# Kernel tuning notes

Measured on AMD Instinct MI355X. Metric: run time of the kernel, lower is better.

## Reference

```python
import jax, jax.numpy as jnp
import numpy as np

B, S, H, NH = 4, 2048, 1024, 16
HD = H // NH  # head_size = 64


def setup_inputs() -> dict:
    key = jax.random.key(0)
    ks = jax.random.split(key, 12)
    s = 1.0 / np.sqrt(H)
    return {
        "query": jax.random.normal(ks[0], (B, S, H), jnp.float32),
        "key": jax.random.normal(ks[1], (B, S, H), jnp.float32),
        "value": jax.random.normal(ks[2], (B, S, H), jnp.float32),
        "attention_mask": jax.random.randint(ks[3], (B, 1, S, S), 0, 2).astype(jnp.float32),
        "Wq": jax.random.normal(ks[4], (H, H), jnp.float32) * s,
        "bq": jnp.zeros((H,), jnp.float32),
        "Wk": jax.random.normal(ks[5], (H, H), jnp.float32) * s,
        "bk": jnp.zeros((H,), jnp.float32),
        "Wv": jax.random.normal(ks[6], (H, H), jnp.float32) * s,
        "bv": jnp.zeros((H,), jnp.float32),
        "Wo": jax.random.normal(ks[7], (H, H), jnp.float32) * s,
        "bo": jnp.zeros((H,), jnp.float32),
    }


def reference(query, key, value, attention_mask, Wq, bq, Wk, bk, Wv, bv, Wo, bo):
    # Linear projections (weights stored [in, out])
    q = query @ Wq + bq   # [B, S, H]
    k = key @ Wk + bk
    v = value @ Wv + bv
    # split heads -> [B, NH, S, HD]
    def heads(x):
        return x.reshape(B, -1, NH, HD).transpose(0, 2, 1, 3)
    q, k, v = heads(q), heads(k), heads(v)
    scale = 1.0 / np.sqrt(HD)
    scores = jnp.einsum("bhqd,bhkd->bhqk", q, k) * scale  # [B, NH, S, S]
    scores = scores + attention_mask * (-1e9)
    attn = jax.nn.softmax(scores, axis=-1)
    # dropout is identity in eval mode (deterministic reference)
    out = jnp.einsum("bhqk,bhkd->bhqd", attn, v)  # [B, NH, S, HD]
    out = out.transpose(0, 2, 1, 3).reshape(B, -1, H)  # [B, S, H]
    return out @ Wo + bo
```

## Files before the change

kernel.cpp:

```cpp
#include <hip/hip_runtime.h>
#include <hip/hip_bf16.h>
#include <stdint.h>

#define B_ 4
#define S_ 2048
#define H_ 1024
#define NH_ 16
#define HD_ 64

typedef __attribute__((ext_vector_type(8))) short short8;
typedef __attribute__((ext_vector_type(4))) float f32x4;
typedef __attribute__((ext_vector_type(4))) unsigned short ushort4v;

__device__ __forceinline__ unsigned short f2bf(float f) {
  union { float f; unsigned u; } x; x.f = f;
  unsigned r = x.u + 0x7fffu + ((x.u >> 16) & 1u);
  return (unsigned short)(r >> 16);
}

#define ALDS16(g, l) \
  __builtin_amdgcn_global_load_lds((const __attribute__((address_space(1))) void*)(g), \
                                   (__attribute__((address_space(3))) void*)(l), 16, 0, 0)

__global__ __launch_bounds__(256) void cvt_in(
    const float* __restrict__ q, const float* __restrict__ k, const float* __restrict__ v,
    unsigned short* __restrict__ oq, unsigned short* __restrict__ ok2, unsigned short* __restrict__ ov) {
  const int z = blockIdx.z;
  const float* src = z == 0 ? q : (z == 1 ? k : v);
  unsigned short* dst = z == 0 ? oq : (z == 1 ? ok2 : ov);
  const size_t i = ((size_t)blockIdx.x * 256 + threadIdx.x) * 8;
  const f32x4 a = *reinterpret_cast<const f32x4*>(src + i);
  const f32x4 c = *reinterpret_cast<const f32x4*>(src + i + 4);
  short8 o;
#pragma unroll
  for (int j = 0; j < 4; ++j) { o[j] = (short)f2bf(a[j]); o[j + 4] = (short)f2bf(c[j]); }
  *reinterpret_cast<short8*>(dst + i) = o;
}

__global__ __launch_bounds__(256) void packmask(
    const float* __restrict__ mask, unsigned long long* __restrict__ mb) {
  const int w = threadIdx.x >> 6, lane = threadIdx.x & 63;
  const int wbase = (blockIdx.x * 4 + w) * 32;
#pragma unroll 8
  for (int i = 0; i < 32; ++i) {
    const float v = mask[(size_t)(wbase + i) * 64 + lane];
    const unsigned long long bits = __ballot(v == 0.0f);
    if (lane == 0) mb[wbase + i] = bits;
  }
}

__global__ __launch_bounds__(256) void cvt_w(
    const float* __restrict__ Wq, const float* __restrict__ Wk,
    const float* __restrict__ Wv, const float* __restrict__ Wo,
    unsigned short* __restrict__ wt) {
  __shared__ float tile[64][65];
  const int z = blockIdx.z;
  const float* W = z == 0 ? Wq : (z == 1 ? Wk : (z == 2 ? Wv : Wo));
  unsigned short* out = wt + (size_t)z * H_ * H_;
  const int t = threadIdx.x;
  const int r0 = blockIdx.y * 64, c0 = blockIdx.x * 64;
  const int tr = t >> 4, tc = (t & 15) * 4;
#pragma unroll
  for (int rr = 0; rr < 4; ++rr) {
    const int row = rr * 16 + tr;
    const f32x4 val = *reinterpret_cast<const f32x4*>(W + (size_t)(r0 + row) * H_ + c0 + tc);
#pragma unroll
    for (int j = 0; j < 4; ++j) tile[row][tc + j] = val[j];
  }
  __syncthreads();
#pragma unroll
  for (int rr = 0; rr < 4; ++rr) {
    const int c = rr * 16 + tr;
    ushort4v o;
#pragma unroll
    for (int j = 0; j < 4; ++j) o[j] = f2bf(tile[tc + j][c]);
    *reinterpret_cast<ushort4v*>(out + (size_t)(c0 + c) * H_ + r0 + tc) = o;
  }
}

template <int OUTMODE>
__device__ __forceinline__ void gemm_body(
    const unsigned short* __restrict__ X, const unsigned short* __restrict__ Wt,
    const float* __restrict__ bias, float oscale, unsigned short* __restrict__ obf,
    float* __restrict__ of32) {
  __shared__ unsigned short As[128 * 64];
  __shared__ unsigned short Bs[128 * 64];
  const int t = threadIdx.x;
  const int w = t >> 6, l = t & 63;
  const int lr = l & 15, lg = l >> 4;
  const int brow = blockIdx.x * 128, bcol = blockIdx.y * 128;
  const int wr = (w >> 1) * 64, wc = (w & 1) * 64;
  f32x4 acc[4][4] = {};
  const unsigned short* xb = X + (size_t)brow * 1024;
  const unsigned short* wb = Wt + (size_t)bcol * 1024;
  int srow[4], skl[4];
#pragma unroll
  for (int j = 0; j < 4; ++j) {
    const int c = t + j * 256;
    srow[j] = c >> 3;
    skl[j] = ((c & 7) ^ ((c >> 3) & 7)) * 8;
  }
  for (int kt = 0; kt < 1024; kt += 64) {
#pragma unroll
    for (int j = 0; j < 4; ++j) {
      ALDS16(xb + (size_t)srow[j] * 1024 + kt + skl[j], As + (t + j * 256) * 8);
      ALDS16(wb + (size_t)srow[j] * 1024 + kt + skl[j], Bs + (t + j * 256) * 8);
    }
    __syncthreads();
#pragma unroll
    for (int kk = 0; kk < 2; ++kk) {
      short8 af[4], bf[4];
#pragma unroll
      for (int m = 0; m < 4; ++m) {
        const int ra = wr + m * 16 + lr;
        af[m] = *reinterpret_cast<const short8*>(As + ra * 64 + ((kk * 4 + lg) ^ (ra & 7)) * 8);
      }
#pragma unroll
      for (int n = 0; n < 4; ++n) {
        const int rb = wc + n * 16 + lr;
        bf[n] = *reinterpret_cast<const short8*>(Bs + rb * 64 + ((kk * 4 + lg) ^ (rb & 7)) * 8);
      }
#pragma unroll
      for (int m = 0; m < 4; ++m)
#pragma unroll
        for (int n = 0; n < 4; ++n)
          acc[m][n] = __builtin_amdgcn_mfma_f32_16x16x32_bf16(af[m], bf[n], acc[m][n], 0, 0, 0);
    }
    __syncthreads();
  }
#pragma unroll
  for (int m = 0; m < 4; ++m) {
#pragma unroll
    for (int n = 0; n < 4; ++n) {
      const int gr0 = brow + wr + m * 16 + lg * 4;
      const int gc = bcol + wc + n * 16 + lr;
      if (OUTMODE == 2) {
        ushort4v o;
#pragma unroll
        for (int r = 0; r < 4; ++r) o[r] = f2bf((acc[m][n][r] + bias[gc]) * oscale);
        const int bb = gr0 >> 11, ss = gr0 & 2047, hh = gc >> 6, dd = gc & 63;
        *reinterpret_cast<ushort4v*>(obf + ((size_t)(bb * NH_ + hh) * HD_ + dd) * S_ + ss) = o;
      } else {
#pragma unroll
        for (int r = 0; r < 4; ++r) {
          const int gr = gr0 + r;
          const float val = (acc[m][n][r] + bias[gc]) * oscale;
          if (OUTMODE == 0) {
            const int bb = gr >> 11, ss = gr & 2047, hh = gc >> 6, dd = gc & 63;
            obf[(((size_t)(bb * NH_ + hh)) * S_ + ss) * HD_ + dd] = f2bf(val);
          } else {
            of32[(size_t)gr * H_ + gc] = val;
          }
        }
      }
    }
  }
}

#define QSCL 0.1803368801111244f

__global__ __launch_bounds__(256, 4) void gemm_qkv(
    const unsigned short* __restrict__ xq, const unsigned short* __restrict__ xk,
    const unsigned short* __restrict__ wt,
    const float* __restrict__ bq, const float* __restrict__ bk,
    unsigned short* __restrict__ qh, unsigned short* __restrict__ kh) {
  const int z = blockIdx.z;
  const unsigned short* X = z == 0 ? xq : xk;
  const unsigned short* W = wt + (size_t)z * H_ * H_;
  const float* bias = z == 0 ? bq : bk;
  unsigned short* out = z == 0 ? qh : kh;
  const float scl = z == 0 ? QSCL : 1.0f;
  gemm_body<0>(X, W, bias, scl, out, nullptr);
}

__global__ __launch_bounds__(256, 4) void gemm_v(
    const unsigned short* __restrict__ xv, const unsigned short* __restrict__ wt,
    const float* __restrict__ bv, unsigned short* __restrict__ vtv) {
  gemm_body<2>(xv, wt + (size_t)2 * H_ * H_, bv, 1.0f, vtv, nullptr);
}

__global__ __launch_bounds__(256, 4) void gemm_out(
    const unsigned short* __restrict__ ao, const unsigned short* __restrict__ wt,
    const float* __restrict__ bo, float* __restrict__ out) {
  gemm_body<1>(ao, wt, bo, 1.0f, nullptr, out);
}

__global__ __launch_bounds__(256, 4) void attn_kernel(
    const unsigned short* __restrict__ qh, const unsigned short* __restrict__ kh,
    const unsigned short* __restrict__ vt, const unsigned long long* __restrict__ mb,
    unsigned short* __restrict__ ao) {
  __shared__ unsigned short Ks[2][64 * 64];
  __shared__ unsigned short Vs[2][64 * 64];
  __shared__ unsigned short Ps[4][16 * 64];
  const int t = threadIdx.x, w = t >> 6, l = t & 63;
  const int lr = l & 15, lg = l >> 4;
  const int flat = blockIdx.x;
  const int xcd = flat & 7;
  const int gen = flat >> 10;
  const int hh = (flat >> 8) & 3;
  const int qt = (flat >> 3) & 31;
  const int bh = gen * 32 + xcd * 4 + hh;
  const int b = bh >> 4, h = bh & 15;
  const unsigned short* qptr = qh + (size_t)bh * S_ * HD_;
  const unsigned short* kptr = kh + (size_t)bh * S_ * HD_;
  const unsigned short* vptr = vt + (size_t)bh * HD_ * S_;
  const unsigned long long* mbase = mb + (size_t)b * S_ * (S_ / 64);
  const int qbase = qt * 64 + w * 16;

  short8 qf[2];
  {
    const unsigned short* qp = qptr + (size_t)(qbase + lr) * HD_ + lg * 8;
    qf[0] = *reinterpret_cast<const short8*>(qp);
    qf[1] = *reinterpret_cast<const short8*>(qp + 32);
  }
  short8 ones;
#pragma unroll
  for (int jj = 0; jj < 8; ++jj) ones[jj] = (short)0x3F80;

  const int si0 = t, si1 = t + 256;
  const int srow0 = si0 >> 3, sk0 = ((si0 & 7) ^ (srow0 & 7)) * 8;
  const int srow1 = si1 >> 3, sk1 = ((si1 & 7) ^ (srow1 & 7)) * 8;
  const unsigned short* ksrc0 = kptr + (size_t)srow0 * HD_ + sk0;
  const unsigned short* ksrc1 = kptr + (size_t)srow1 * HD_ + sk1;
  const unsigned short* vsrc0 = vptr + (size_t)srow0 * S_ + sk0;
  const unsigned short* vsrc1 = vptr + (size_t)srow1 * S_ + sk1;
  size_t moff[4];
#pragma unroll
  for (int r = 0; r < 4; ++r)
    moff[r] = (size_t)(qbase + lg * 4 + r) * (S_ / 64);

  ALDS16(ksrc0, Ks[0] + si0 * 8);
  ALDS16(ksrc1, Ks[0] + si1 * 8);
  ALDS16(vsrc0, Vs[0] + si0 * 8);
  ALDS16(vsrc1, Vs[0] + si1 * 8);
  __syncthreads();

  f32x4 acc_o[4] = {};
  f32x4 acc_l = {};
  unsigned short* pw = Ps[w];
  int cur = 0;

  for (int kv = 0; kv < S_; kv += 64) {
    unsigned msel[4][4];
#pragma unroll
    for (int r = 0; r < 4; ++r) {
      const unsigned long long mwv = mbase[moff[r] + (kv >> 6)];
      const unsigned long long sh = mwv >> lr;
      const unsigned lo = (unsigned)sh, hi = (unsigned)(sh >> 32);
      msel[r][0] = 0u - (lo & 1u);
      msel[r][1] = 0u - ((lo >> 16) & 1u);
      msel[r][2] = 0u - (hi & 1u);
      msel[r][3] = 0u - ((hi >> 16) & 1u);
    }

    const int nkv = (kv + 64 < S_) ? kv + 64 : 0;
    ALDS16(ksrc0 + (size_t)nkv * HD_, Ks[cur ^ 1] + si0 * 8);
    ALDS16(ksrc1 + (size_t)nkv * HD_, Ks[cur ^ 1] + si1 * 8);
    ALDS16(vsrc0 + nkv, Vs[cur ^ 1] + si0 * 8);
    ALDS16(vsrc1 + nkv, Vs[cur ^ 1] + si1 * 8);

    const unsigned short* Kc = Ks[cur];
    const unsigned short* Vc = Vs[cur];

    float p[4][4];
#pragma unroll
    for (int n = 0; n < 4; ++n) {
      const int krow = n * 16 + lr;
      const short8 kf0 = *reinterpret_cast<const short8*>(Kc + krow * 64 + ((0 + lg) ^ (krow & 7)) * 8);
      const short8 kf1 = *reinterpret_cast<const short8*>(Kc + krow * 64 + ((4 + lg) ^ (krow & 7)) * 8);
      f32x4 sc = {};
      sc = __builtin_amdgcn_mfma_f32_16x16x32_bf16(qf[0], kf0, sc, 0, 0, 0);
      sc = __builtin_amdgcn_mfma_f32_16x16x32_bf16(qf[1], kf1, sc, 0, 0, 0);
#pragma unroll
      for (int r = 0; r < 4; ++r) {
        union { float f; unsigned u; } cv;
        cv.f = __builtin_amdgcn_exp2f(sc[r]);
        cv.u &= msel[r][n];
        p[n][r] = cv.f;
      }
    }

#pragma unroll
    for (int r = 0; r < 4; ++r) {
      const int row = lg * 4 + r;
#pragma unroll
      for (int n = 0; n < 4; ++n) {
        union { float f; unsigned u; } cv; cv.f = p[n][r];
        const int col = n * 16 + lr;
        pw[row * 64 + ((col >> 3) ^ (row & 7)) * 8 + (col & 7)] = (unsigned short)(cv.u >> 16);
      }
    }
    short8 pf0 = *reinterpret_cast<const short8*>(pw + lr * 64 + ((0 + lg) ^ (lr & 7)) * 8);
    short8 pf1 = *reinterpret_cast<const short8*>(pw + lr * 64 + ((4 + lg) ^ (lr & 7)) * 8);
    acc_l = __builtin_amdgcn_mfma_f32_16x16x32_bf16(pf0, ones, acc_l, 0, 0, 0);
    acc_l = __builtin_amdgcn_mfma_f32_16x16x32_bf16(pf1, ones, acc_l, 0, 0, 0);

    __builtin_amdgcn_s_setprio(1);
#pragma unroll
    for (int d = 0; d < 4; ++d) {
      const int vrow = d * 16 + lr;
      const short8 vf0 = *reinterpret_cast<const short8*>(Vc + vrow * 64 + ((0 + lg) ^ (vrow & 7)) * 8);
      const short8 vf1 = *reinterpret_cast<const short8*>(Vc + vrow * 64 + ((4 + lg) ^ (vrow & 7)) * 8);
      acc_o[d] = __builtin_amdgcn_mfma_f32_16x16x32_bf16(pf0, vf0, acc_o[d], 0, 0, 0);
      acc_o[d] = __builtin_amdgcn_mfma_f32_16x16x32_bf16(pf1, vf1, acc_o[d], 0, 0, 0);
    }
    __builtin_amdgcn_s_setprio(0);
    __syncthreads();
    cur ^= 1;
  }

#pragma unroll
  for (int r = 0; r < 4; ++r) {
    const float inv = __builtin_amdgcn_rcpf(acc_l[r]);
    const int qrow = qbase + lg * 4 + r;
    unsigned short* orow = ao + ((size_t)b * S_ + qrow) * H_ + h * HD_;
#pragma unroll
    for (int d = 0; d < 4; ++d)
      orow[d * 16 + lr] = f2bf(acc_o[d][r] * inv);
  }
}

extern "C" void kernel_launch(void* const* d_in, const int* in_sizes, int n_in,
                              void* d_out, int out_size, void* d_ws, size_t ws_size,
                              hipStream_t stream) {
  (void)in_sizes; (void)n_in; (void)out_size; (void)ws_size;
  const float* query = (const float*)d_in[0];
  const float* key_  = (const float*)d_in[1];
  const float* value = (const float*)d_in[2];
  const float* mask  = (const float*)d_in[3];
  const float* Wq = (const float*)d_in[4];
  const float* bq = (const float*)d_in[5];
  const float* Wk = (const float*)d_in[6];
  const float* bk = (const float*)d_in[7];
  const float* Wv = (const float*)d_in[8];
  const float* bv = (const float*)d_in[9];
  const float* Wo = (const float*)d_in[10];
  const float* bo = (const float*)d_in[11];
  float* out = (float*)d_out;

  char* ws = (char*)d_ws;
  const size_t MB16 = (size_t)1 << 24;
  unsigned short* XQ = (unsigned short*)(ws + 0 * MB16);
  unsigned short* XK = (unsigned short*)(ws + 1 * MB16);
  unsigned short* XV = (unsigned short*)(ws + 2 * MB16);
  unsigned short* QH = (unsigned short*)(ws + 3 * MB16);
  unsigned short* KH = (unsigned short*)(ws + 4 * MB16);
  unsigned short* VT = (unsigned short*)(ws + 5 * MB16);
  unsigned short* WT = (unsigned short*)(ws + 6 * MB16);
  unsigned long long* MBits = (unsigned long long*)(ws + 6 * MB16 + (size_t)4 * H_ * H_ * 2);
  unsigned short* AO = XQ;

  cvt_in<<<dim3(4096, 1, 3), 256, 0, stream>>>(query, key_, value, XQ, XK, XV);
  packmask<<<dim3(2048), 256, 0, stream>>>(mask, MBits);
  cvt_w<<<dim3(16, 16, 4), 256, 0, stream>>>(Wq, Wk, Wv, Wo, WT);
  gemm_qkv<<<dim3(64, 8, 2), 256, 0, stream>>>(XQ, XK, WT, bq, bk, QH, KH);
  gemm_v<<<dim3(64, 8), 256, 0, stream>>>(XV, WT, bv, VT);
  attn_kernel<<<dim3(2048), 256, 0, stream>>>(QH, KH, VT, MBits, AO);
  gemm_out<<<dim3(64, 8, 1), 256, 0, stream>>>(AO, WT + 3 * (size_t)H_ * H_, bo, out);
}
```

Measured before the change: 257.0 us.

## Merge Q/K/V projection GEMMs into one launch and prefetch mask words

Replaces the separate QK and V projection launches with one kernel over a 24-wide y grid. The weight column offset comes from blockIdx.y, and bias and head indices are masked to stay within range. The attention kernel also loads the next tile's packed mask words one iteration early, overlapping that latency with compute, and simplifies the bit extraction. The fused launch removes one kernel launch and its tail, but adds a branch to the GEMM and relies on gemm_body indexing weights by blockIdx.y.

```diff
diff --git a/kernel.cpp b/kernel.cpp
--- a/kernel.cpp
+++ b/kernel.cpp
@@ -137,16 +137,16 @@
       if (OUTMODE == 2) {
         ushort4v o;
 #pragma unroll
-        for (int r = 0; r < 4; ++r) o[r] = f2bf((acc[m][n][r] + bias[gc]) * oscale);
-        const int bb = gr0 >> 11, ss = gr0 & 2047, hh = gc >> 6, dd = gc & 63;
+        for (int r = 0; r < 4; ++r) o[r] = f2bf((acc[m][n][r] + bias[gc & 1023]) * oscale);
+        const int bb = gr0 >> 11, ss = gr0 & 2047, hh = (gc >> 6) & 15, dd = gc & 63;
         *reinterpret_cast<ushort4v*>(obf + ((size_t)(bb * NH_ + hh) * HD_ + dd) * S_ + ss) = o;
       } else {
 #pragma unroll
         for (int r = 0; r < 4; ++r) {
           const int gr = gr0 + r;
-          const float val = (acc[m][n][r] + bias[gc]) * oscale;
+          const float val = (acc[m][n][r] + bias[gc & 1023]) * oscale;
           if (OUTMODE == 0) {
-            const int bb = gr >> 11, ss = gr & 2047, hh = gc >> 6, dd = gc & 63;
+            const int bb = gr >> 11, ss = gr & 2047, hh = (gc >> 6) & 15, dd = gc & 63;
             obf[(((size_t)(bb * NH_ + hh)) * S_ + ss) * HD_ + dd] = f2bf(val);
           } else {
             of32[(size_t)gr * H_ + gc] = val;
@@ -159,24 +159,16 @@
 
 #define QSCL 0.1803368801111244f
 
-__global__ __launch_bounds__(256, 4) void gemm_qkv(
+__global__ __launch_bounds__(256, 4) void gemm_qkvf(
     const unsigned short* __restrict__ xq, const unsigned short* __restrict__ xk,
-    const unsigned short* __restrict__ wt,
-    const float* __restrict__ bq, const float* __restrict__ bk,
-    unsigned short* __restrict__ qh, unsigned short* __restrict__ kh) {
-  const int z = blockIdx.z;
-  const unsigned short* X = z == 0 ? xq : xk;
-  const unsigned short* W = wt + (size_t)z * H_ * H_;
-  const float* bias = z == 0 ? bq : bk;
-  unsigned short* out = z == 0 ? qh : kh;
-  const float scl = z == 0 ? QSCL : 1.0f;
-  gemm_body<0>(X, W, bias, scl, out, nullptr);
-}
-
-__global__ __launch_bounds__(256, 4) void gemm_v(
     const unsigned short* __restrict__ xv, const unsigned short* __restrict__ wt,
-    const float* __restrict__ bv, unsigned short* __restrict__ vtv) {
-  gemm_body<2>(xv, wt + (size_t)2 * H_ * H_, bv, 1.0f, vtv, nullptr);
+    const float* __restrict__ bq, const float* __restrict__ bk, const float* __restrict__ bv,
+    unsigned short* __restrict__ qh, unsigned short* __restrict__ kh,
+    unsigned short* __restrict__ vtv) {
+  const int seg = blockIdx.y >> 3;
+  if (seg == 0)      gemm_body<0>(xq, wt, bq, QSCL, qh, nullptr);
+  else if (seg == 1) gemm_body<0>(xk, wt, bk, 1.0f, kh, nullptr);
+  else               gemm_body<2>(xv, wt, bv, 1.0f, vtv, nullptr);
 }
 
 __global__ __launch_bounds__(256, 4) void gemm_out(
@@ -194,6 +186,7 @@
   __shared__ unsigned short Ps[4][16 * 64];
   const int t = threadIdx.x, w = t >> 6, l = t & 63;
   const int lr = l & 15, lg = l >> 4;
+  const int lr16 = lr + 16;
   const int flat = blockIdx.x;
   const int xcd = flat & 7;
   const int gen = flat >> 10;
@@ -233,6 +226,9 @@
   ALDS16(ksrc1, Ks[0] + si1 * 8);
   ALDS16(vsrc0, Vs[0] + si0 * 8);
   ALDS16(vsrc1, Vs[0] + si1 * 8);
+  unsigned long long mwv[4];
+#pragma unroll
+  for (int r = 0; r < 4; ++r) mwv[r] = mbase[moff[r]];
   __syncthreads();
 
   f32x4 acc_o[4] = {};
@@ -244,13 +240,11 @@
     unsigned msel[4][4];
 #pragma unroll
     for (int r = 0; r < 4; ++r) {
-      const unsigned long long mwv = mbase[moff[r] + (kv >> 6)];
-      const unsigned long long sh = mwv >> lr;
-      const unsigned lo = (unsigned)sh, hi = (unsigned)(sh >> 32);
-      msel[r][0] = 0u - (lo & 1u);
-      msel[r][1] = 0u - ((lo >> 16) & 1u);
-      msel[r][2] = 0u - (hi & 1u);
-      msel[r][3] = 0u - ((hi >> 16) & 1u);
+      const unsigned lo = (unsigned)mwv[r], hi = (unsigned)(mwv[r] >> 32);
+      msel[r][0] = 0u - ((lo >> lr) & 1u);
+      msel[r][1] = 0u - ((lo >> lr16) & 1u);
+      msel[r][2] = 0u - ((hi >> lr) & 1u);
+      msel[r][3] = 0u - ((hi >> lr16) & 1u);
     }
 
     const int nkv = (kv + 64 < S_) ? kv + 64 : 0;
@@ -258,6 +252,8 @@
     ALDS16(ksrc1 + (size_t)nkv * HD_, Ks[cur ^ 1] + si1 * 8);
     ALDS16(vsrc0 + nkv, Vs[cur ^ 1] + si0 * 8);
     ALDS16(vsrc1 + nkv, Vs[cur ^ 1] + si1 * 8);
+#pragma unroll
+    for (int r = 0; r < 4; ++r) mwv[r] = mbase[moff[r] + (nkv >> 6)];
 
     const unsigned short* Kc = Ks[cur];
     const unsigned short* Vc = Vs[cur];
@@ -353,8 +349,7 @@
   cvt_in<<<dim3(4096, 1, 3), 256, 0, stream>>>(query, key_, value, XQ, XK, XV);
   packmask<<<dim3(2048), 256, 0, stream>>>(mask, MBits);
   cvt_w<<<dim3(16, 16, 4), 256, 0, stream>>>(Wq, Wk, Wv, Wo, WT);
-  gemm_qkv<<<dim3(64, 8, 2), 256, 0, stream>>>(XQ, XK, WT, bq, bk, QH, KH);
-  gemm_v<<<dim3(64, 8), 256, 0, stream>>>(XV, WT, bv, VT);
+  gemm_qkvf<<<dim3(64, 24), 256, 0, stream>>>(XQ, XK, XV, WT, bq, bk, bv, QH, KH, VT);
   attn_kernel<<<dim3(2048), 256, 0, stream>>>(QH, KH, VT, MBits, AO);
-  gemm_out<<<dim3(64, 8, 1), 256, 0, stream>>>(AO, WT + 3 * (size_t)H_ * H_, bo, out);
-}
+  gemm_out<<<dim3(64, 8), 256, 0, stream>>>(AO, WT + 3 * (size_t)H_ * H_, bo, out);
+}
```

New measurement: 267.2 us. 1.04x slower.

## Rewrite attention with 32x32 MFMA tiles and register-only P transposition

Applied to the files above, without the earlier changes.

The attention kernel now runs 2 waves of 32 query rows each, using 32x32x16 bf16 MFMAs with S computed transposed (K as A operand), so the softmax probabilities land in registers in a layout that can feed the PV MFMA directly. The per-wave LDS round trip for P is replaced by packed bf16 conversion plus permlane32 swaps (or shuffles as a fallback), and mask bits are read with one 64-bit load per lane instead of four. This removes LDS traffic and a store/load dependency on every KV step and raises the MFMA shape, but halves threads per block. That means each thread issues more async K/V loads and holds larger f32x16 accumulators, which increases register pressure and can lower occupancy.

```diff
diff --git a/kernel.cpp b/kernel.cpp
--- a/kernel.cpp
+++ b/kernel.cpp
@@ -10,12 +10,20 @@
 
 typedef __attribute__((ext_vector_type(8))) short short8;
 typedef __attribute__((ext_vector_type(4))) float f32x4;
+typedef __attribute__((ext_vector_type(16))) float f32x16;
 typedef __attribute__((ext_vector_type(4))) unsigned short ushort4v;
+typedef __attribute__((ext_vector_type(2))) unsigned uint2v;
 
 __device__ __forceinline__ unsigned short f2bf(float f) {
   union { float f; unsigned u; } x; x.f = f;
   unsigned r = x.u + 0x7fffu + ((x.u >> 16) & 1u);
   return (unsigned short)(r >> 16);
+}
+
+__device__ __forceinline__ unsigned cvtpk_bf16(float a, float b) {
+  unsigned r;
+  asm("v_cvt_pk_bf16_f32 %0, %1, %2" : "=v"(r) : "v"(a), "v"(b));
+  return r;
 }
 
 #define ALDS16(g, l) \
@@ -185,15 +193,22 @@
   gemm_body<1>(ao, wt, bo, 1.0f, nullptr, out);
 }
 
-__global__ __launch_bounds__(256, 4) void attn_kernel(
+#if defined(__has_builtin)
+#if __has_builtin(__builtin_amdgcn_permlane32_swap)
+#define HAVE_PLSWAP 1
+#endif
+#endif
+
+__global__ __launch_bounds__(128, 2) void attn_kernel(
     const unsigned short* __restrict__ qh, const unsigned short* __restrict__ kh,
     const unsigned short* __restrict__ vt, const unsigned long long* __restrict__ mb,
     unsigned short* __restrict__ ao) {
-  __shared__ unsigned short Ks[2][64 * 64];
-  __shared__ unsigned short Vs[2][64 * 64];
-  __shared__ unsigned short Ps[4][16 * 64];
-  const int t = threadIdx.x, w = t >> 6, l = t & 63;
-  const int lr = l & 15, lg = l >> 4;
+  constexpr int KSZ = 64 * 64 + 256;
+  __shared__ unsigned short Ks[2][KSZ];
+  __shared__ unsigned short Vs[2][KSZ];
+  const int t = threadIdx.x, l = t & 63, w = t >> 6;
+  const int lq = l & 31;
+  const int lg = l >> 5;
   const int flat = blockIdx.x;
   const int xcd = flat & 7;
   const int gen = flat >> 10;
@@ -205,104 +220,119 @@
   const unsigned short* kptr = kh + (size_t)bh * S_ * HD_;
   const unsigned short* vptr = vt + (size_t)bh * HD_ * S_;
   const unsigned long long* mbase = mb + (size_t)b * S_ * (S_ / 64);
-  const int qbase = qt * 64 + w * 16;
-
-  short8 qf[2];
+  const int qbase = qt * 64 + w * 32;
+
+  short8 qreg[4];
   {
-    const unsigned short* qp = qptr + (size_t)(qbase + lr) * HD_ + lg * 8;
-    qf[0] = *reinterpret_cast<const short8*>(qp);
-    qf[1] = *reinterpret_cast<const short8*>(qp + 32);
+    const unsigned short* qp = qptr + (size_t)(qbase + lq) * HD_ + lg * 8;
+#pragma unroll
+    for (int ks = 0; ks < 4; ++ks)
+      qreg[ks] = *reinterpret_cast<const short8*>(qp + ks * 16);
   }
   short8 ones;
 #pragma unroll
   for (int jj = 0; jj < 8; ++jj) ones[jj] = (short)0x3F80;
 
-  const int si0 = t, si1 = t + 256;
-  const int srow0 = si0 >> 3, sk0 = ((si0 & 7) ^ (srow0 & 7)) * 8;
-  const int srow1 = si1 >> 3, sk1 = ((si1 & 7) ^ (srow1 & 7)) * 8;
-  const unsigned short* ksrc0 = kptr + (size_t)srow0 * HD_ + sk0;
-  const unsigned short* ksrc1 = kptr + (size_t)srow1 * HD_ + sk1;
-  const unsigned short* vsrc0 = vptr + (size_t)srow0 * S_ + sk0;
-  const unsigned short* vsrc1 = vptr + (size_t)srow1 * S_ + sk1;
-  size_t moff[4];
-#pragma unroll
-  for (int r = 0; r < 4; ++r)
-    moff[r] = (size_t)(qbase + lg * 4 + r) * (S_ / 64);
-
-  ALDS16(ksrc0, Ks[0] + si0 * 8);
-  ALDS16(ksrc1, Ks[0] + si1 * 8);
-  ALDS16(vsrc0, Vs[0] + si0 * 8);
-  ALDS16(vsrc1, Vs[0] + si1 * 8);
+  int srow[4], skl[4];
+#pragma unroll
+  for (int j = 0; j < 4; ++j) {
+    const int c = t + j * 128;
+    srow[j] = c >> 3;
+    skl[j] = ((c & 7) ^ ((c >> 3) & 7)) * 8;
+  }
+  const size_t moff = (size_t)(qbase + lq) * (S_ / 64);
+
+#pragma unroll
+  for (int j = 0; j < 4; ++j) {
+    ALDS16(kptr + (size_t)srow[j] * HD_ + skl[j], Ks[0] + (t + j * 128) * 8);
+    ALDS16(vptr + (size_t)srow[j] * S_ + skl[j], Vs[0] + (t + j * 128) * 8);
+  }
   __syncthreads();
 
-  f32x4 acc_o[4] = {};
-  f32x4 acc_l = {};
-  unsigned short* pw = Ps[w];
+  f32x16 acc_o0 = {}, acc_o1 = {}, acc_l = {};
   int cur = 0;
 
   for (int kv = 0; kv < S_; kv += 64) {
-    unsigned msel[4][4];
-#pragma unroll
-    for (int r = 0; r < 4; ++r) {
-      const unsigned long long mwv = mbase[moff[r] + (kv >> 6)];
-      const unsigned long long sh = mwv >> lr;
-      const unsigned lo = (unsigned)sh, hi = (unsigned)(sh >> 32);
-      msel[r][0] = 0u - (lo & 1u);
-      msel[r][1] = 0u - ((lo >> 16) & 1u);
-      msel[r][2] = 0u - (hi & 1u);
-      msel[r][3] = 0u - ((hi >> 16) & 1u);
-    }
+    const unsigned long long mwv = mbase[moff + (kv >> 6)];
 
     const int nkv = (kv + 64 < S_) ? kv + 64 : 0;
-    ALDS16(ksrc0 + (size_t)nkv * HD_, Ks[cur ^ 1] + si0 * 8);
-    ALDS16(ksrc1 + (size_t)nkv * HD_, Ks[cur ^ 1] + si1 * 8);
-    ALDS16(vsrc0 + nkv, Vs[cur ^ 1] + si0 * 8);
-    ALDS16(vsrc1 + nkv, Vs[cur ^ 1] + si1 * 8);
+#pragma unroll
+    for (int j = 0; j < 4; ++j) {
+      ALDS16(kptr + (size_t)(nkv + srow[j]) * HD_ + skl[j], Ks[cur ^ 1] + (t + j * 128) * 8);
+      ALDS16(vptr + (size_t)srow[j] * S_ + nkv + skl[j], Vs[cur ^ 1] + (t + j * 128) * 8);
+    }
 
     const unsigned short* Kc = Ks[cur];
     const unsigned short* Vc = Vs[cur];
 
-    float p[4][4];
-#pragma unroll
-    for (int n = 0; n < 4; ++n) {
-      const int krow = n * 16 + lr;
-      const short8 kf0 = *reinterpret_cast<const short8*>(Kc + krow * 64 + ((0 + lg) ^ (krow & 7)) * 8);
-      const short8 kf1 = *reinterpret_cast<const short8*>(Kc + krow * 64 + ((4 + lg) ^ (krow & 7)) * 8);
-      f32x4 sc = {};
-      sc = __builtin_amdgcn_mfma_f32_16x16x32_bf16(qf[0], kf0, sc, 0, 0, 0);
-      sc = __builtin_amdgcn_mfma_f32_16x16x32_bf16(qf[1], kf1, sc, 0, 0, 0);
-#pragma unroll
-      for (int r = 0; r < 4; ++r) {
-        union { float f; unsigned u; } cv;
-        cv.f = __builtin_amdgcn_exp2f(sc[r]);
-        cv.u &= msel[r][n];
-        p[n][r] = cv.f;
-      }
-    }
-
-#pragma unroll
-    for (int r = 0; r < 4; ++r) {
-      const int row = lg * 4 + r;
-#pragma unroll
-      for (int n = 0; n < 4; ++n) {
-        union { float f; unsigned u; } cv; cv.f = p[n][r];
-        const int col = n * 16 + lr;
-        pw[row * 64 + ((col >> 3) ^ (row & 7)) * 8 + (col & 7)] = (unsigned short)(cv.u >> 16);
-      }
-    }
-    short8 pf0 = *reinterpret_cast<const short8*>(pw + lr * 64 + ((0 + lg) ^ (lr & 7)) * 8);
-    short8 pf1 = *reinterpret_cast<const short8*>(pw + lr * 64 + ((4 + lg) ^ (lr & 7)) * 8);
-    acc_l = __builtin_amdgcn_mfma_f32_16x16x32_bf16(pf0, ones, acc_l, 0, 0, 0);
-    acc_l = __builtin_amdgcn_mfma_f32_16x16x32_bf16(pf1, ones, acc_l, 0, 0, 0);
+    f32x16 s0 = {}, s1 = {};
+#pragma unroll
+    for (int ks = 0; ks < 4; ++ks) {
+      const short8 kf0 = *reinterpret_cast<const short8*>(
+          Kc + lq * 64 + (((ks * 2 + lg) ^ (lq & 7)) * 8));
+      s0 = __builtin_amdgcn_mfma_f32_32x32x16_bf16(kf0, qreg[ks], s0, 0, 0, 0);
+    }
+#pragma unroll
+    for (int ks = 0; ks < 4; ++ks) {
+      const short8 kf1 = *reinterpret_cast<const short8*>(
+          Kc + (32 + lq) * 64 + (((ks * 2 + lg) ^ (lq & 7)) * 8));
+      s1 = __builtin_amdgcn_mfma_f32_32x32x16_bf16(kf1, qreg[ks], s1, 0, 0, 0);
+    }
+
+    const unsigned sh0 = (unsigned)(mwv >> (lg * 4));
+    const unsigned sh1 = (unsigned)(mwv >> (32 + lg * 4));
+    float p0[16], p1[16];
+#pragma unroll
+    for (int r = 0; r < 16; ++r) {
+      const int pos = (r & 3) + 8 * (r >> 2);
+      union { float f; unsigned u; } c0, c1;
+      c0.f = __builtin_amdgcn_exp2f(s0[r]);
+      c0.u &= (0u - ((sh0 >> pos) & 1u));
+      p0[r] = c0.f;
+      c1.f = __builtin_amdgcn_exp2f(s1[r]);
+      c1.u &= (0u - ((sh1 >> pos) & 1u));
+      p1[r] = c1.f;
+    }
+
+    short8 pfrag[4];
+#pragma unroll
+    for (int ks2 = 0; ks2 < 4; ++ks2) {
+      const float* pt = (ks2 >> 1) ? p1 : p0;
+      const int base = (ks2 & 1) * 8;
+      const unsigned pkA = cvtpk_bf16(pt[base + 0], pt[base + 1]);
+      const unsigned pkB = cvtpk_bf16(pt[base + 2], pt[base + 3]);
+      const unsigned pkC = cvtpk_bf16(pt[base + 4], pt[base + 5]);
+      const unsigned pkD = cvtpk_bf16(pt[base + 6], pt[base + 7]);
+      union { unsigned u[4]; short8 s; } fr;
+#ifdef HAVE_PLSWAP
+      const uint2v r02 = __builtin_amdgcn_permlane32_swap(pkA, pkC, false, false);
+      const uint2v r13 = __builtin_amdgcn_permlane32_swap(pkB, pkD, false, false);
+      fr.u[0] = r02[0]; fr.u[1] = r13[0]; fr.u[2] = r02[1]; fr.u[3] = r13[1];
+#else
+      const unsigned pA_sw = (unsigned)__shfl_xor((int)pkA, 32);
+      const unsigned pB_sw = (unsigned)__shfl_xor((int)pkB, 32);
+      const unsigned pC_sw = (unsigned)__shfl_xor((int)pkC, 32);
+      const unsigned pD_sw = (unsigned)__shfl_xor((int)pkD, 32);
+      fr.u[0] = lg ? pC_sw : pkA;
+      fr.u[1] = lg ? pD_sw : pkB;
+      fr.u[2] = lg ? pkC : pA_sw;
+      fr.u[3] = lg ? pkD : pB_sw;
+#endif
+      pfrag[ks2] = fr.s;
+    }
 
     __builtin_amdgcn_s_setprio(1);
 #pragma unroll
-    for (int d = 0; d < 4; ++d) {
-      const int vrow = d * 16 + lr;
-      const short8 vf0 = *reinterpret_cast<const short8*>(Vc + vrow * 64 + ((0 + lg) ^ (vrow & 7)) * 8);
-      const short8 vf1 = *reinterpret_cast<const short8*>(Vc + vrow * 64 + ((4 + lg) ^ (vrow & 7)) * 8);
-      acc_o[d] = __builtin_amdgcn_mfma_f32_16x16x32_bf16(pf0, vf0, acc_o[d], 0, 0, 0);
-      acc_o[d] = __builtin_amdgcn_mfma_f32_16x16x32_bf16(pf1, vf1, acc_o[d], 0, 0, 0);
+    for (int ks2 = 0; ks2 < 4; ++ks2)
+      acc_l = __builtin_amdgcn_mfma_f32_32x32x16_bf16(pfrag[ks2], ones, acc_l, 0, 0, 0);
+#pragma unroll
+    for (int ks2 = 0; ks2 < 4; ++ks2) {
+      const short8 vf0 = *reinterpret_cast<const short8*>(
+          Vc + lq * 64 + (((ks2 * 2 + lg) ^ (lq & 7)) * 8));
+      acc_o0 = __builtin_amdgcn_mfma_f32_32x32x16_bf16(pfrag[ks2], vf0, acc_o0, 0, 0, 0);
+      const short8 vf1 = *reinterpret_cast<const short8*>(
+          Vc + (32 + lq) * 64 + (((ks2 * 2 + lg) ^ (lq & 7)) * 8));
+      acc_o1 = __builtin_amdgcn_mfma_f32_32x32x16_bf16(pfrag[ks2], vf1, acc_o1, 0, 0, 0);
     }
     __builtin_amdgcn_s_setprio(0);
     __syncthreads();
@@ -310,13 +340,12 @@
   }
 
 #pragma unroll
-  for (int r = 0; r < 4; ++r) {
+  for (int r = 0; r < 16; ++r) {
+    const int qrow = qbase + (r & 3) + 8 * (r >> 2) + 4 * lg;
     const float inv = __builtin_amdgcn_rcpf(acc_l[r]);
-    const int qrow = qbase + lg * 4 + r;
-    unsigned short* orow = ao + ((size_t)b * S_ + qrow) * H_ + h * HD_;
-#pragma unroll
-    for (int d = 0; d < 4; ++d)
-      orow[d * 16 + lr] = f2bf(acc_o[d][r] * inv);
+    unsigned short* orow = ao + ((size_t)b * S_ + qrow) * H_ + h * HD_ + lq;
+    orow[0] = f2bf(acc_o0[r] * inv);
+    orow[32] = f2bf(acc_o1[r] * inv);
   }
 }
 
@@ -355,6 +384,6 @@
   cvt_w<<<dim3(16, 16, 4), 256, 0, stream>>>(Wq, Wk, Wv, Wo, WT);
   gemm_qkv<<<dim3(64, 8, 2), 256, 0, stream>>>(XQ, XK, WT, bq, bk, QH, KH);
   gemm_v<<<dim3(64, 8), 256, 0, stream>>>(XV, WT, bv, VT);
-  attn_kernel<<<dim3(2048), 256, 0, stream>>>(QH, KH, VT, MBits, AO);
-  gemm_out<<<dim3(64, 8, 1), 256, 0, stream>>>(AO, WT + 3 * (size_t)H_ * H_, bo, out);
-}
+  attn_kernel<<<dim3(2048), 128, 0, stream>>>(QH, KH, VT, MBits, AO);
+  gemm_out<<<dim3(64, 8), 256, 0, stream>>>(AO, WT + 3 * (size_t)H_ * H_, bo, out);
+}
```

New measurement: 273.6 us. +6.5%, slower.
